# Optimization experiments

Hardware: AMD Instinct MI355X
Metric: run time of the kernel (lower is better)

## Reference

```python
import jax, jax.numpy as jnp
import numpy as np

# B docs, N total nodes (E entities + M mentions + S sentences), R relation types, H heads
B, N, E, M, S, D, IN, R, H = 8, 224, 64, 128, 32, 256, 300, 5, 4


def setup_inputs() -> dict:
    key = jax.random.key(0)
    ks = jax.random.split(key, 24)
    p = lambda k, shp: jax.random.normal(k, shp, dtype=jnp.float32) * 0.05
    return {
        "nodes": jax.random.normal(ks[0], (B, N, IN), dtype=jnp.float32),
        "adj": (jax.random.uniform(ks[1], (B, R, N, N)) < 0.05).astype(jnp.float32),
        "mentions": jax.random.normal(ks[2], (B, M, D), dtype=jnp.float32),
        "sentences": jax.random.normal(ks[3], (B * S, D), dtype=jnp.float32),
        "Wr0": p(ks[4], (R, IN, D)), "br0": p(ks[5], (R, D)),
        "Wr1": p(ks[6], (R, D, D)), "br1": p(ks[7], (R, D)),
        "W00": p(ks[8], (IN, D)), "b00": p(ks[9], (D,)),
        "W01": p(ks[10], (D, D)), "b01": p(ks[11], (D,)),
        "Wq_h": p(ks[12], (D, D)), "Wk_h": p(ks[13], (D, D)),
        "Wv_h": p(ks[14], (D, D)), "Wo_h": p(ks[15], (D, D)),
        "Wq_t": p(ks[16], (D, D)), "Wk_t": p(ks[17], (D, D)),
        "Wv_t": p(ks[18], (D, D)), "Wo_t": p(ks[19], (D, D)),
        # entity id (local, 0..E-1) of each mention: each entity owns M/E=2 mentions
        "info_eid": (jnp.arange(B * M, dtype=jnp.int32) % E).reshape(B, M),
        # flat sentence index of each mention, within its own doc's sentence block
        "info_sid": jax.random.randint(ks[20], (B, M), 0, S, dtype=jnp.int32)
        + jnp.arange(B, dtype=jnp.int32)[:, None] * S,
    }


def _mha(key_t, value_t, query_t, mask, Wq, Wk, Wv, Wo):
    # mask: [B, P, M], True = exclude (mention does not belong to the masked entity)
    b, p, d = query_t.shape
    m = key_t.shape[1]
    dk = d // H
    Q = (query_t @ Wq).reshape(b, p, H, dk)
    K = (key_t @ Wk).reshape(b, m, H, dk)
    V = (value_t @ Wv).reshape(b, m, H, dk)
    s = jnp.einsum("bphk,bmhk->bhpm", Q, K) / jnp.sqrt(jnp.asarray(dk, Q.dtype))
    s = jnp.where(mask[:, None, :, :], jnp.asarray(-1e9, s.dtype), s)
    a = jax.nn.softmax(s, axis=-1)
    ctx = jnp.einsum("bhpm,bmhk->bphk", a, V).reshape(b, p, d)
    return ctx @ Wo


def reference(nodes, adj, mentions, sentences, Wr0, br0, Wr1, br1, W00, b00,
              W01, b01, Wq_h, Wk_h, Wv_h, Wo_h, Wq_t, Wk_t, Wv_t, Wo_t,
              info_eid, info_sid):
    # ---- RGCN_Layer: per-relation message passing, degree-normalized ----
    # denom: in-degree per node summed over relations, +1 (matches torch.sparse.sum dim=1)
    denoms = adj.sum(axis=3).sum(axis=1)[..., None] + 1.0  # [B, N, 1]

    def rgcn_layer(x, Wr, br, W0, b0):
        xW = jnp.einsum("bni,rid->brnd", x, Wr) + br[None, :, None, :]  # [B,R,N,D]
        AxW = jnp.einsum("brnm,brmd->bnd", adj, xW)  # aggregate + sum over relations
        return jax.nn.relu((AxW + x @ W0 + b0) / denoms)

    h = rgcn_layer(nodes, Wr0, br0, W00, b00)
    gcn_out = rgcn_layer(h, Wr1, br1, W01, b01)  # [B, N, D] global node reps

    # ---- Local_rep_layer: masked pairwise multi-head attention ----
    ents = gcn_out[:, :E, :]  # query='global': entities = global nodes (first E rows)
    # pair (i, j): query_1 -> entity i, query_2 -> entity j
    q1 = jnp.broadcast_to(ents[:, :, None, :], (B, E, E, D)).reshape(B, E * E, D)
    q2 = jnp.broadcast_to(ents[:, None, :, :], (B, E, E, D)).reshape(B, E * E, D)
    mention_sen_rep = sentences[info_sid]  # F.embedding(info[:,4], sentences) -> [B,M,D]
    # index_m[b, e, m] True iff mention m does NOT belong to entity e
    index_m = info_eid[:, None, :] != jnp.arange(E, dtype=info_eid.dtype)[None, :, None]
    mask_h = jnp.broadcast_to(index_m[:, :, None, :], (B, E, E, M)).reshape(B, E * E, M)
    mask_t = jnp.broadcast_to(index_m[:, None, :, :], (B, E, E, M)).reshape(B, E * E, M)
    rep_h = _mha(mention_sen_rep, mentions, q2, mask_h, Wq_h, Wk_h, Wv_h, Wo_h)
    rep_t = _mha(mention_sen_rep, mentions, q1, mask_t, Wq_t, Wk_t, Wv_t, Wo_t)
    # concatenate outputs along node axis for a single return array
    return jnp.concatenate([gcn_out, rep_h, rep_t], axis=1)  # [B, N + 2*E*E, D]
```

## Files before the change

### kernel.cpp

```cpp
#include <hip/hip_runtime.h>
#include <math.h>

#define B_ 8
#define N_ 224
#define E_ 64
#define M_ 128
#define S_ 32
#define D_ 256
#define IN_ 300
#define R_ 5
#define H_ 4
#define DK_ 64
#define OUTROWS (N_ + 2 * E_ * E_)
#define CAP_ 192
#define BN_ (B_ * N_)

typedef __attribute__((ext_vector_type(8))) short bf16x8;
typedef __attribute__((ext_vector_type(8))) unsigned short u16x8;
typedef __attribute__((ext_vector_type(4))) float f32x4;

__device__ inline short f2bf(float f) {
    union { float f; unsigned u; } x; x.f = f;
    unsigned u = x.u;
    unsigned r = (u + 0x7fffu + ((u >> 16) & 1u)) >> 16;
    return (short)r;
}
__device__ inline float bf2f(unsigned short s) {
    union { unsigned u; float f; } x; x.u = ((unsigned)s) << 16; return x.f;
}

__device__ inline void gload16(const void* g, void* l) {
    __builtin_amdgcn_global_load_lds(
        (const __attribute__((address_space(1))) unsigned int*)g,
        (__attribute__((address_space(3))) unsigned int*)l, 16, 0, 0);
}

#define PRE_PACK 1376
#define PRE_EDGE (PRE_PACK + BN_)
#define PRE_ML   (PRE_EDGE + 2)
#define CVT_N    573440
#define CVT_M    262144
#define PRE_TOT  (PRE_ML + 1072)

__global__ __launch_bounds__(256) void mega_pre(
    short* __restrict__ Wb,
    const float* Wr0, const float* W00, const float* Wr1, const float* W01,
    const float* Wkh, const float* Wkt, const float* Wvh, const float* Wvt,
    const float* Wqh, const float* Wqt, const float* Woh, const float* Wot,
    const float* __restrict__ adj, int* __restrict__ ecnt, int* __restrict__ elist,
    float* __restrict__ evals, float* __restrict__ den,
    const int* __restrict__ eid, int* __restrict__ mcnt, int* __restrict__ mlist,
    const float* __restrict__ nodes, const float* __restrict__ mentions,
    const float* __restrict__ sentences, const int* __restrict__ sid,
    short* __restrict__ nodesb, short* __restrict__ mentb, short* __restrict__ msrb) {
    __shared__ int smemi[528];
    __shared__ int wtot[4];
    __shared__ float wsum[4];
    int blk = blockIdx.x, tid = threadIdx.x;

    if (blk < PRE_PACK) {
        short (*T)[33] = (short(*)[33])smemi;
        int t = blk;
        const float* src; short* outp; int outld, klim, n0, k0;
        if (t < 480) {
            int z = t / 80, tt = t % 80;
            n0 = (tt & 7) * 32; k0 = (tt >> 3) * 32;
            outp = Wb + (size_t)z * 81920; outld = 320; klim = IN_;
            src = (z < 5) ? Wr0 + (size_t)z * IN_ * D_ : W00;
        } else if (t < 864) {
            int l = t - 480, z = l / 64, tt = l % 64;
            n0 = (tt & 7) * 32; k0 = (tt >> 3) * 32;
            outp = Wb + 491520 + (size_t)z * 65536; outld = 256; klim = 256;
            src = (z < 5) ? Wr1 + (size_t)z * D_ * D_ : W01;
        } else if (t < 992) {
            int l = t - 864, z = l / 64, tt = l % 64;
            n0 = (tt & 7) * 32; k0 = (tt >> 3) * 32;
            outp = Wb + 884736 + (size_t)z * 65536; outld = 256; klim = 256;
            src = z ? Wkt : Wkh;
        } else if (t < 1120) {
            int l = t - 992, z = l / 64, tt = l % 64;
            n0 = (tt & 7) * 32; k0 = (tt >> 3) * 32;
            outp = Wb + 1146880 + (size_t)z * 65536; outld = 256; klim = 256;
            src = z ? Wvt : Wvh;
        } else if (t < 1248) {
            int l = t - 1120, z = l / 64, tt = l % 64;
            n0 = (tt & 7) * 32; k0 = (tt >> 3) * 32;
            outp = Wb + 1409024 + (size_t)z * 65536; outld = 256; klim = 256;
            src = z ? Wqt : Wqh;
        } else {
            int l = t - 1248, z = l / 16, tt = l % 16;
            n0 = (tt & 7) * 32; k0 = (tt >> 3) * 32;
            outp = Wb + 1671168 + (size_t)z * 16384; outld = 64; klim = 64;
            int which = z >> 2, h = z & 3;
            src = (which ? Wot : Woh) + (size_t)(h * 64) * D_;
        }
        int tx = tid & 31, ty = tid >> 5;
#pragma unroll
        for (int i = 0; i < 4; ++i) {
            int k = k0 + ty + 8 * i;
            float v = (k < klim) ? src[(size_t)k * D_ + n0 + tx] : 0.f;
            T[tx][ty + 8 * i] = f2bf(v);
        }
        __syncthreads();
#pragma unroll
        for (int i = 0; i < 4; ++i) {
            int n = ty + 8 * i;
            outp[(size_t)(n0 + n) * outld + k0 + tx] = T[n][tx];
        }
    } else if (blk < PRE_EDGE) {
        int bn = blk - PRE_PACK;
        int b = bn / N_, n = bn % N_;
        int lane = tid & 63, wv4 = tid >> 6;
        int idxs[5]; float vals[5];
        int cloc = 0; float sloc = 0.f;
        for (int e = tid; e < R_ * N_; e += 256) {
            int r = e / N_, m = e % N_;
            float v = adj[(((size_t)(b * R_ + r)) * N_ + n) * N_ + m];
            if (v != 0.f) { idxs[cloc] = e; vals[cloc] = v; ++cloc; sloc += v; }
        }
        int v = cloc;
#pragma unroll
        for (int st = 1; st < 64; st <<= 1) {
            int o = __shfl_up(v, st, 64);
            if (lane >= st) v += o;
        }
        float fs = sloc;
#pragma unroll
        for (int st = 32; st > 0; st >>= 1) fs += __shfl_xor(fs, st, 64);
        if (lane == 63) wtot[wv4] = v;
        if (lane == 0)  wsum[wv4] = fs;
        __syncthreads();
        int woff = 0;
        for (int i = 0; i < wv4; ++i) woff += wtot[i];
        int off = woff + v - cloc;
        int total = wtot[0] + wtot[1] + wtot[2] + wtot[3];
        size_t base = (size_t)bn * CAP_;
        for (int i = 0; i < cloc; ++i) {
            int p = off + i;
            if (p < CAP_) { elist[base + p] = idxs[i]; evals[base + p] = vals[i]; }
        }
        if (tid == 0) {
            ecnt[bn] = total < CAP_ ? total : CAP_;
            den[bn] = wsum[0] + wsum[1] + wsum[2] + wsum[3] + 1.0f;
        }
    } else if (blk < PRE_ML) {
        int t = (blk - PRE_EDGE) * 256 + tid;
        if (t < B_ * E_) {
            int b = t / E_, i = t % E_;
            int c = 0;
            for (int m = 0; m < M_; ++m)
                if (eid[b * M_ + m] == i) mlist[(size_t)t * M_ + c++] = m;
            mcnt[t] = c;
        }
    } else {
        int idx = (blk - PRE_ML) * 1024 + tid * 4;
#pragma unroll
        for (int j = 0; j < 4; ++j) {
            int i = idx + j;
            if (i < CVT_N) {
                int row = i / 320, k = i % 320;
                nodesb[i] = (k < IN_) ? f2bf(nodes[(size_t)row * IN_ + k]) : (short)0;
            } else if (i < CVT_N + CVT_M) {
                int i2 = i - CVT_N;
                mentb[i2] = f2bf(mentions[i2]);
            } else {
                int i3 = i - CVT_N - CVT_M;
                int bm = i3 >> 8, d = i3 & 255;
                msrb[i3] = f2bf(sentences[(size_t)sid[bm] * D_ + d]);
            }
        }
    }
}

__global__ __launch_bounds__(256) void axw_gather(
    const short* __restrict__ xWb,
    const int* __restrict__ ecnt, const int* __restrict__ elist,
    const float* __restrict__ evals, const float* __restrict__ den,
    short* __restrict__ hb, float* __restrict__ out, long long out_bstride,
    short* __restrict__ entsb) {
    int bn = blockIdx.x;
    int b = bn / N_, n = bn % N_;
    int tid = threadIdx.x, wv = tid >> 6, dq = tid & 63;
    int c = ecnt[bn];
    const int* lst = elist + (size_t)bn * CAP_;
    const float* vls = evals + (size_t)bn * CAP_;
    float4 acc = make_float4(0.f, 0.f, 0.f, 0.f);
#pragma unroll 2
    for (int k = wv; k < c; k += 4) {
        int e = lst[k];
        float v = vls[k];
        int r = e / N_, m = e % N_;
        ushort4 x4 = *(const ushort4*)&xWb[((size_t)(r * BN_ + b * N_ + m)) * 256 + dq * 4];
        acc.x += v * bf2f(x4.x); acc.y += v * bf2f(x4.y);
        acc.z += v * bf2f(x4.z); acc.w += v * bf2f(x4.w);
    }
    __shared__ float4 red[4][64];
    red[wv][dq] = acc;
    __syncthreads();
    if (tid < 64) {
        float4 s0 = red[0][dq], s1 = red[1][dq], s2 = red[2][dq], s3 = red[3][dq];
        ushort4 t4 = *(const ushort4*)&xWb[((size_t)(5 * BN_ + bn)) * 256 + dq * 4];
        float inv = 1.f / den[bn];
        float4 o;
        o.x = fmaxf((s0.x + s1.x + s2.x + s3.x + bf2f(t4.x)) * inv, 0.f);
        o.y = fmaxf((s0.y + s1.y + s2.y + s3.y + bf2f(t4.y)) * inv, 0.f);
        o.z = fmaxf((s0.z + s1.z + s2.z + s3.z + bf2f(t4.z)) * inv, 0.f);
        o.w = fmaxf((s0.w + s1.w + s2.w + s3.w + bf2f(t4.w)) * inv, 0.f);
        if (hb) {
            ushort4 hw = { (unsigned short)f2bf(o.x), (unsigned short)f2bf(o.y),
                           (unsigned short)f2bf(o.z), (unsigned short)f2bf(o.w) };
            *(ushort4*)&hb[(size_t)bn * 256 + dq * 4] = hw;
        }
        if (out)
            *(float4*)&out[(size_t)b * out_bstride + (size_t)n * 256 + dq * 4] = o;
        if (entsb && n < E_) {
            ushort4 ew = { (unsigned short)f2bf(o.x), (unsigned short)f2bf(o.y),
                           (unsigned short)f2bf(o.z), (unsigned short)f2bf(o.w) };
            *(ushort4*)&entsb[((size_t)b * E_ + n) * 256 + dq * 4] = ew;
        }
    }
}

struct GDesc {
    const short* A; const short* Bt; short* C; const float* bias;
    int lda, ldbk, ldc, Kloop, ny;
};
struct GTable { GDesc d[24]; };

__global__ __launch_bounds__(256) void gemm_multi(GTable T) {
    GDesc g = T.d[blockIdx.z];
    if ((int)blockIdx.y >= g.ny) return;

    __shared__ short As[64 * 64];
    __shared__ short Bs[64 * 64];
    int tid = threadIdx.x;
    int lane = tid & 63, wv = tid >> 6;
    int wr = wv >> 1, wc = wv & 1;
    int fr = lane & 15;
    int so = lane >> 4;
    int row0 = blockIdx.y * 64, col0 = blockIdx.x * 64;

    int l8 = lane >> 3;
    int sl = (lane & 7) ^ l8;
    int c0 = 2 * wv, c1 = c0 + 1;
    int ra0 = row0 + 8 * c0 + l8, ra1 = row0 + 8 * c1 + l8;
    int rb0 = col0 + 8 * c0 + l8, rb1 = col0 + 8 * c1 + l8;

    f32x4 acc00 = {0.f,0.f,0.f,0.f}, acc01 = acc00, acc10 = acc00, acc11 = acc00;

    int rA0 = wr * 32 + fr, rA1 = rA0 + 16;
    int rB0 = wc * 32 + fr, rB1 = rB0 + 16;
    int sw = fr & 7;

    for (int k0 = 0; k0 < g.Kloop; k0 += 64) {
        gload16(&g.A [(size_t)ra0 * g.lda  + k0 + sl * 8], &As[c0 * 512]);
        gload16(&g.A [(size_t)ra1 * g.lda  + k0 + sl * 8], &As[c1 * 512]);
        gload16(&g.Bt[(size_t)rb0 * g.ldbk + k0 + sl * 8], &Bs[c0 * 512]);
        gload16(&g.Bt[(size_t)rb1 * g.ldbk + k0 + sl * 8], &Bs[c1 * 512]);
        __syncthreads();
#pragma unroll
        for (int ks = 0; ks < 2; ++ks) {
            int s = ks * 4 + so;
            bf16x8 a0 = *(bf16x8*)&As[rA0 * 64 + ((s ^ sw) << 3)];
            bf16x8 a1 = *(bf16x8*)&As[rA1 * 64 + ((s ^ sw) << 3)];
            bf16x8 b0 = *(bf16x8*)&Bs[rB0 * 64 + ((s ^ sw) << 3)];
            bf16x8 b1 = *(bf16x8*)&Bs[rB1 * 64 + ((s ^ sw) << 3)];
            acc00 = __builtin_amdgcn_mfma_f32_16x16x32_bf16(a0, b0, acc00, 0, 0, 0);
            acc01 = __builtin_amdgcn_mfma_f32_16x16x32_bf16(a0, b1, acc01, 0, 0, 0);
            acc10 = __builtin_amdgcn_mfma_f32_16x16x32_bf16(a1, b0, acc10, 0, 0, 0);
            acc11 = __builtin_amdgcn_mfma_f32_16x16x32_bf16(a1, b1, acc11, 0, 0, 0);
        }
        __syncthreads();
    }

    int rbase = row0 + wr * 32 + (lane >> 4) * 4;
    int cbase = col0 + wc * 32 + fr;
    f32x4 accs[2][2] = {{acc00, acc01}, {acc10, acc11}};
#pragma unroll
    for (int mi = 0; mi < 2; ++mi) {
#pragma unroll
        for (int nj = 0; nj < 2; ++nj) {
            int cc = cbase + nj * 16;
            float bval = g.bias ? g.bias[cc] : 0.f;
#pragma unroll
            for (int r = 0; r < 4; ++r) {
                int cr = rbase + mi * 16 + r;
                g.C[(size_t)cr * g.ldc + cc] = f2bf(accs[mi][nj][r] + bval);
            }
        }
    }
}

__device__ inline float dot64_bf(const short* q, const short* k) {
    float dot = 0.f;
#pragma unroll
    for (int t8 = 0; t8 < 8; ++t8) {
        u16x8 qv = *(const u16x8*)(q + t8 * 8);
        u16x8 kv = *(const u16x8*)(k + t8 * 8);
#pragma unroll
        for (int j = 0; j < 8; ++j) dot += bf2f(qv[j]) * bf2f(kv[j]);
    }
    return dot;
}

__global__ __launch_bounds__(256) void combine_kernel(
    const short* __restrict__ Qb, const short* __restrict__ Kb,
    const short* __restrict__ VWb, const int* __restrict__ cnt,
    const int* __restrict__ mlist, float* __restrict__ out) {
    int z = blockIdx.z;
    const short* Q  = Qb  + (size_t)z * (B_ * E_ * D_);
    const short* K  = Kb  + (size_t)z * (B_ * M_ * D_);
    const short* VW = VWb + (size_t)z * (B_ * M_ * H_ * D_);
    int baserow = N_ + z * (E_ * E_);
    int me = blockIdx.x;
    int b = blockIdx.y;
    int tid = threadIdx.x;
    int dq = tid & 63;
    __shared__ float sVW[2][H_ * D_];
    __shared__ float sS[E_][H_][2];
    int c = cnt[b * E_ + me];
    const int* lst = mlist + (size_t)(b * E_ + me) * M_;

    if (c >= 1 && c <= 2) {
        for (int k = 0; k < c; ++k) {
            ushort4 v4 = *(const ushort4*)(VW + ((size_t)b * M_ + lst[k]) * (H_ * D_) + tid * 4);
            *(float4*)&sVW[k][tid * 4] =
                make_float4(bf2f(v4.x), bf2f(v4.y), bf2f(v4.z), bf2f(v4.w));
        }
        for (int e = tid; e < E_ * H_ * 2; e += 256) {
            int k = e & 1, hh = (e >> 1) & 3, ql = e >> 3;
            if (k < c) {
                const short* Qrow = Q + ((size_t)b * E_ + ql) * D_ + hh * DK_;
                const short* Krow = K + ((size_t)b * M_ + lst[k]) * D_ + hh * DK_;
                sS[ql][hh][k] = dot64_bf(Qrow, Krow) * 0.125f;
            }
        }
        __syncthreads();
        {
            int hh = tid & 3, ql = tid >> 2;
            float mx = sS[ql][hh][0];
            for (int k = 1; k < c; ++k) mx = fmaxf(mx, sS[ql][hh][k]);
            float w[2]; float sm = 0.f;
            for (int k = 0; k < c; ++k) { w[k] = __expf(sS[ql][hh][k] - mx); sm += w[k]; }
            float inv = 1.f / sm;
            for (int k = 0; k < c; ++k) sS[ql][hh][k] = w[k] * inv;
        }
        __syncthreads();
        for (int qq = tid >> 6; qq < E_; qq += 4) {
            float4 acc = make_float4(0.f, 0.f, 0.f, 0.f);
#pragma unroll
            for (int hh = 0; hh < H_; ++hh)
                for (int k = 0; k < c; ++k) {
                    float w = sS[qq][hh][k];
                    float4 v = *(const float4*)&sVW[k][hh * D_ + dq * 4];
                    acc.x += w * v.x; acc.y += w * v.y; acc.z += w * v.z; acc.w += w * v.w;
                }
            int row = z ? (qq * E_ + me) : (me * E_ + qq);
            *(float4*)&out[((size_t)b * OUTROWS + baserow + row) * D_ + dq * 4] = acc;
        }
    } else if (c == 0) {
        float s = 0.f;
        for (int m = 0; m < M_; ++m)
            for (int hh = 0; hh < H_; ++hh)
                s += bf2f((unsigned short)VW[((size_t)b * M_ + m) * (H_ * D_) + hh * D_ + tid]);
        sVW[0][tid] = s * (1.0f / M_);
        __syncthreads();
        for (int qq = tid >> 6; qq < E_; qq += 4) {
            float4 v = *(const float4*)&sVW[0][dq * 4];
            int row = z ? (qq * E_ + me) : (me * E_ + qq);
            *(float4*)&out[((size_t)b * OUTROWS + baserow + row) * D_ + dq * 4] = v;
        }
    } else {
        {
            int hh = tid & 3, ql = tid >> 2;
            const short* Qrow = Q + ((size_t)b * E_ + ql) * D_ + hh * DK_;
            float mx = -1e30f;
            for (int k = 0; k < c; ++k) {
                const short* Krow = K + ((size_t)b * M_ + lst[k]) * D_ + hh * DK_;
                mx = fmaxf(mx, dot64_bf(Qrow, Krow) * 0.125f);
            }
            float sm = 0.f;
            for (int k = 0; k < c; ++k) {
                const short* Krow = K + ((size_t)b * M_ + lst[k]) * D_ + hh * DK_;
                sm += __expf(dot64_bf(Qrow, Krow) * 0.125f - mx);
            }
            sS[ql][hh][0] = mx;
            sS[ql][hh][1] = sm;
        }
        __syncthreads();
        for (int qq = tid >> 6; qq < E_; qq += 4) {
            float4 acc = make_float4(0.f, 0.f, 0.f, 0.f);
            for (int hh = 0; hh < H_; ++hh) {
                float mx = sS[qq][hh][0], inv = 1.f / sS[qq][hh][1];
                const short* Qrow = Q + ((size_t)b * E_ + qq) * D_ + hh * DK_;
                for (int k = 0; k < c; ++k) {
                    const short* Krow = K + ((size_t)b * M_ + lst[k]) * D_ + hh * DK_;
                    float w = __expf(dot64_bf(Qrow, Krow) * 0.125f - mx) * inv;
                    ushort4 v4 = *(const ushort4*)(VW + ((size_t)b * M_ + lst[k]) * (H_ * D_) + hh * D_ + dq * 4);
                    acc.x += w * bf2f(v4.x); acc.y += w * bf2f(v4.y);
                    acc.z += w * bf2f(v4.z); acc.w += w * bf2f(v4.w);
                }
            }
            int row = z ? (qq * E_ + me) : (me * E_ + qq);
            *(float4*)&out[((size_t)b * OUTROWS + baserow + row) * D_ + dq * 4] = acc;
        }
    }
}

extern "C" void kernel_launch(void* const* d_in, const int* in_sizes, int n_in,
                              void* d_out, int out_size, void* d_ws, size_t ws_size,
                              hipStream_t stream) {
    const float* nodes     = (const float*)d_in[0];
    const float* adj       = (const float*)d_in[1];
    const float* mentions  = (const float*)d_in[2];
    const float* sentences = (const float*)d_in[3];
    const float* Wr0 = (const float*)d_in[4];
    const float* br0 = (const float*)d_in[5];
    const float* Wr1 = (const float*)d_in[6];
    const float* br1 = (const float*)d_in[7];
    const float* W00 = (const float*)d_in[8];
    const float* b00 = (const float*)d_in[9];
    const float* W01 = (const float*)d_in[10];
    const float* b01 = (const float*)d_in[11];
    const float* Wq_h = (const float*)d_in[12];
    const float* Wk_h = (const float*)d_in[13];
    const float* Wv_h = (const float*)d_in[14];
    const float* Wo_h = (const float*)d_in[15];
    const float* Wq_t = (const float*)d_in[16];
    const float* Wk_t = (const float*)d_in[17];
    const float* Wv_t = (const float*)d_in[18];
    const float* Wo_t = (const float*)d_in[19];
    const int* info_eid = (const int*)d_in[20];
    const int* info_sid = (const int*)d_in[21];
    float* out  = (float*)d_out;
    float* pool = (float*)d_ws;

    short* xWb   = (short*)pool;
    short* VWb   = (short*)pool;
    short* Qb    = (short*)(pool + 1048576);
    short* hb    = (short*)(pool + 1376256);
    short* entsb = (short*)(pool + 1605632);
    short* KVb   = (short*)(pool + 1671168);
    short* nodesb= (short*)(pool + 2195456);
    short* msrb  = (short*)(pool + 2482176);
    short* mentb = (short*)(pool + 2613248);
    short* Wb    = (short*)(pool + 2744320);
    int*   elist = (int*)(pool + 3645440);
    float* evals = pool + 3989504;
    int*   ecnt  = (int*)(pool + 4333568);
    float* den   = pool + 4335360;
    int*   mcnt  = (int*)(pool + 4337152);
    int*   mlist = (int*)(pool + 4337664);

    short* W1t = Wb;
    short* W2t = Wb + 491520;
    short* WKt = Wb + 884736;
    short* WVt = Wb + 1146880;
    short* WQt = Wb + 1409024;
    short* WOt = Wb + 1671168;

    mega_pre<<<PRE_TOT, 256, 0, stream>>>(
        Wb, Wr0, W00, Wr1, W01, Wk_h, Wk_t, Wv_h, Wv_t, Wq_h, Wq_t, Wo_h, Wo_t,
        adj, ecnt, elist, evals, den, info_eid, mcnt, mlist,
        nodes, mentions, sentences, info_sid, nodesb, mentb, msrb);

    {
        GTable T = {};
        for (int z = 0; z < 6; ++z)
            T.d[z] = { nodesb, W1t + z * 81920, xWb + (size_t)z * BN_ * D_,
                       (z < 5) ? br0 + z * D_ : b00, 320, 320, D_, 320, 28 };
        for (int zp = 0; zp < 4; ++zp) {
            int half = zp >> 1, wt = zp & 1;
            T.d[6 + zp] = { msrb + half * 262144, (half ? WVt : WKt) + wt * 65536,
                            KVb + half * 524288 + wt * 262144,
                            nullptr, D_, D_, D_, D_, 16 };
        }
        gemm_multi<<<dim3(4, 28, 10), 256, 0, stream>>>(T);
    }
    axw_gather<<<BN_, 256, 0, stream>>>(xWb, ecnt, elist, evals, den,
                                        hb, nullptr, 0, nullptr);
    {
        GTable T = {};
        for (int z = 0; z < 6; ++z)
            T.d[z] = { hb, W2t + z * 65536, xWb + (size_t)z * BN_ * D_,
                       (z < 5) ? br1 + z * D_ : b01, D_, D_, D_, D_, 28 };
        gemm_multi<<<dim3(4, 28, 6), 256, 0, stream>>>(T);
    }
    axw_gather<<<BN_, 256, 0, stream>>>(xWb, ecnt, elist, evals, den,
                                        nullptr, out, (long long)OUTROWS * D_, entsb);
    {
        GTable T = {};
        for (int zp = 0; zp < 8; ++zp) {
            int which = zp >> 2, hh = zp & 3;
            T.d[zp] = { KVb + 524288 + which * 262144 + hh * DK_,
                        WOt + which * 65536 + hh * 16384,
                        VWb + (size_t)which * (B_ * M_ * H_ * D_) + hh * D_,
                        nullptr, D_, DK_, H_ * D_, DK_, 16 };
        }
        for (int z = 0; z < 16; ++z) {
            int b = z >> 1, which = z & 1;
            T.d[8 + z] = { entsb + b * 16384, WQt + which * 65536,
                           Qb + which * 131072 + b * 16384,
                           nullptr, D_, D_, D_, D_, 1 };
        }
        gemm_multi<<<dim3(4, 16, 24), 256, 0, stream>>>(T);
    }
    combine_kernel<<<dim3(E_, B_, 2), 256, 0, stream>>>(Qb, KVb, VWb, mcnt, mlist, out);
}
```

Baseline: 100.1 us.

## Fuse entity Q projection into gather and merge VW GEMM into layer-2 launch

The entity query projection (ents @ Wq for both heads) now runs inside the second axw_gather kernel as a per-row dot product against the bf16 weights, so the separate entsb buffer and its GEMM tiles go away. The Wv·Wo per-head GEMMs are folded into the layer-2 gemm_multi launch, which removes one kernel launch, and VWb/Qb move to new workspace offsets to avoid aliasing with xWb. The cost is that 64 of every 224 gather blocks now do a 256x512 scalar-FMA projection with uncoalesced per-thread weight rows.

```diff
diff --git a/kernel.cpp b/kernel.cpp
--- a/kernel.cpp
+++ b/kernel.cpp
@@ -177,7 +177,7 @@
     const int* __restrict__ ecnt, const int* __restrict__ elist,
     const float* __restrict__ evals, const float* __restrict__ den,
     short* __restrict__ hb, float* __restrict__ out, long long out_bstride,
-    short* __restrict__ entsb) {
+    const short* __restrict__ WQ, short* __restrict__ qout) {
     int bn = blockIdx.x;
     int b = bn / N_, n = bn % N_;
     int tid = threadIdx.x, wv = tid >> 6, dq = tid & 63;
@@ -195,6 +195,7 @@
         acc.z += v * bf2f(x4.z); acc.w += v * bf2f(x4.w);
     }
     __shared__ float4 red[4][64];
+    __shared__ float rowsh[256];
     red[wv][dq] = acc;
     __syncthreads();
     if (tid < 64) {
@@ -213,11 +214,27 @@
         }
         if (out)
             *(float4*)&out[(size_t)b * out_bstride + (size_t)n * 256 + dq * 4] = o;
-        if (entsb && n < E_) {
-            ushort4 ew = { (unsigned short)f2bf(o.x), (unsigned short)f2bf(o.y),
-                           (unsigned short)f2bf(o.z), (unsigned short)f2bf(o.w) };
-            *(ushort4*)&entsb[((size_t)b * E_ + n) * 256 + dq * 4] = ew;
-        }
+        *(float4*)&rowsh[dq * 4] = o;
+    }
+    if (qout && n < E_) {
+        __syncthreads();
+        const short* wc0 = WQ + (size_t)tid * 256;
+        const short* wc1 = WQ + 65536 + (size_t)tid * 256;
+        float d0 = 0.f, d1 = 0.f;
+#pragma unroll 4
+        for (int k8 = 0; k8 < 256; k8 += 8) {
+            u16x8 w0 = *(const u16x8*)(wc0 + k8);
+            u16x8 w1 = *(const u16x8*)(wc1 + k8);
+#pragma unroll
+            for (int j = 0; j < 8; ++j) {
+                float rv = rowsh[k8 + j];
+                d0 += rv * bf2f(w0[j]);
+                d1 += rv * bf2f(w1[j]);
+            }
+        }
+        size_t qoff = ((size_t)b * E_ + n) * 256 + tid;
+        qout[qoff] = f2bf(d0);
+        qout[131072 + qoff] = f2bf(d1);
     }
 }
 
@@ -225,7 +242,7 @@
     const short* A; const short* Bt; short* C; const float* bias;
     int lda, ldbk, ldc, Kloop, ny;
 };
-struct GTable { GDesc d[24]; };
+struct GTable { GDesc d[14]; };
 
 __global__ __launch_bounds__(256) void gemm_multi(GTable T) {
     GDesc g = T.d[blockIdx.z];
@@ -436,10 +453,7 @@
     float* pool = (float*)d_ws;
 
     short* xWb   = (short*)pool;
-    short* VWb   = (short*)pool;
-    short* Qb    = (short*)(pool + 1048576);
     short* hb    = (short*)(pool + 1376256);
-    short* entsb = (short*)(pool + 1605632);
     short* KVb   = (short*)(pool + 1671168);
     short* nodesb= (short*)(pool + 2195456);
     short* msrb  = (short*)(pool + 2482176);
@@ -451,6 +465,8 @@
     float* den   = pool + 4335360;
     int*   mcnt  = (int*)(pool + 4337152);
     int*   mlist = (int*)(pool + 4337664);
+    short* VWb   = (short*)(pool + 4403200);
+    short* Qb    = (short*)(pool + 5451776);
 
     short* W1t = Wb;
     short* W2t = Wb + 491520;
@@ -478,32 +494,22 @@
         gemm_multi<<<dim3(4, 28, 10), 256, 0, stream>>>(T);
     }
     axw_gather<<<BN_, 256, 0, stream>>>(xWb, ecnt, elist, evals, den,
-                                        hb, nullptr, 0, nullptr);
+                                        hb, nullptr, 0, nullptr, nullptr);
     {
         GTable T = {};
         for (int z = 0; z < 6; ++z)
             T.d[z] = { hb, W2t + z * 65536, xWb + (size_t)z * BN_ * D_,
                        (z < 5) ? br1 + z * D_ : b01, D_, D_, D_, D_, 28 };
-        gemm_multi<<<dim3(4, 28, 6), 256, 0, stream>>>(T);
-    }
-    axw_gather<<<BN_, 256, 0, stream>>>(xWb, ecnt, elist, evals, den,
-                                        nullptr, out, (long long)OUTROWS * D_, entsb);
-    {
-        GTable T = {};
         for (int zp = 0; zp < 8; ++zp) {
             int which = zp >> 2, hh = zp & 3;
-            T.d[zp] = { KVb + 524288 + which * 262144 + hh * DK_,
-                        WOt + which * 65536 + hh * 16384,
-                        VWb + (size_t)which * (B_ * M_ * H_ * D_) + hh * D_,
-                        nullptr, D_, DK_, H_ * D_, DK_, 16 };
-        }
-        for (int z = 0; z < 16; ++z) {
-            int b = z >> 1, which = z & 1;
-            T.d[8 + z] = { entsb + b * 16384, WQt + which * 65536,
-                           Qb + which * 131072 + b * 16384,
-                           nullptr, D_, D_, D_, D_, 1 };
-        }
-        gemm_multi<<<dim3(4, 16, 24), 256, 0, stream>>>(T);
-    }
+            T.d[6 + zp] = { KVb + 524288 + which * 262144 + hh * DK_,
+                            WOt + which * 65536 + hh * 16384,
+                            VWb + (size_t)which * (B_ * M_ * H_ * D_) + hh * D_,
+                            nullptr, D_, DK_, H_ * D_, DK_, 16 };
+        }
+        gemm_multi<<<dim3(4, 28, 14), 256, 0, stream>>>(T);
+    }
+    axw_gather<<<BN_, 256, 0, stream>>>(xWb, ecnt, elist, evals, den,
+                                        nullptr, out, (long long)OUTROWS * D_, WQt, Qb);
     combine_kernel<<<dim3(E_, B_, 2), 256, 0, stream>>>(Qb, KVb, VWb, mcnt, mlist, out);
 }
```

Result: slower. 106.0 us (+5.9%).
